# Kernel tuning notes

Hardware: AMD Instinct MI355X
Metric: run time of the kernel (lower is better)

## Reference

```python
import jax, jax.numpy as jnp
import numpy as np

T, B = 32, 64
D_IN = 512      # input_size == embedding dim
H = 512         # hidden_size
V = 32000       # n_vocab
F_FEAT = 768    # feature_size
NH = 8          # num_heads
HD = H // NH    # head_dim


def setup_inputs() -> dict:
    key = jax.random.key(0)
    ks = jax.random.split(key, 16)
    s = 0.02
    inp = {
        'y': jax.random.randint(ks[0], (T, B), 0, V),
        'ctx': jax.random.normal(ks[1], (1, B, F_FEAT), jnp.float32),
        'emb_W': jax.random.normal(ks[2], (V, D_IN), jnp.float32) * s,
        # GRUCell dec0: gates ordered (r, z, n) as in torch
        'W_ih': jax.random.normal(ks[3], (3 * H, D_IN), jnp.float32) * s,
        'b_ih': jnp.zeros((3 * H,), jnp.float32),
        'W_hh': jax.random.normal(ks[4], (3 * H, H), jnp.float32) * s,
        'b_hh': jnp.zeros((3 * H,), jnp.float32),
        # FF att: feature_size -> hidden, tanh
        'W_att': jax.random.normal(ks[5], (H, F_FEAT), jnp.float32) * s,
        'b_att': jnp.zeros((H,), jnp.float32),
        # MultiHeadSelfAttention projections (hidden -> hidden)
        'Wq': jax.random.normal(ks[6], (H, H), jnp.float32) * s,
        'bq': jnp.zeros((H,), jnp.float32),
        'Wk': jax.random.normal(ks[7], (H, H), jnp.float32) * s,
        'bk': jnp.zeros((H,), jnp.float32),
        'Wv': jax.random.normal(ks[8], (H, H), jnp.float32) * s,
        'bv': jnp.zeros((H,), jnp.float32),
        'Wfc': jax.random.normal(ks[9], (H, H), jnp.float32) * s,
        'bfc': jnp.zeros((H,), jnp.float32),
        # FF hid2out: hidden -> input, tanh, bias_zero
        'W_h2o': jax.random.normal(ks[10], (D_IN, H), jnp.float32) * s,
        'b_h2o': jnp.zeros((D_IN,), jnp.float32),
        # FF out2prob: input -> vocab, linear
        'W_out': jax.random.normal(ks[11], (V, D_IN), jnp.float32) * s,
        'b_out': jnp.zeros((V,), jnp.float32),
    }
    return inp


def reference(y, ctx, emb_W, W_ih, b_ih, W_hh, b_hh, W_att, b_att,
              Wq, bq, Wk, bk, Wv, bv, Wfc, bfc, W_h2o, b_h2o, W_out, b_out):
    y_emb = emb_W[y]                                   # [T, B, D_IN]
    # ct is constant across decode steps: tanh FF over pooled image feature
    ct = jnp.tanh(ctx[0] @ W_att.T + b_att)            # [B, H]
    h0 = jnp.zeros((y.shape[1], H), y_emb.dtype)       # dec_init 'zero'

    def step(h, y_t):
        # torch GRUCell (gate order r, z, n)
        gi = y_t @ W_ih.T + b_ih                       # [B, 3H]
        gh = h @ W_hh.T + b_hh                         # [B, 3H]
        gi_r, gi_z, gi_n = jnp.split(gi, 3, axis=-1)
        gh_r, gh_z, gh_n = jnp.split(gh, 3, axis=-1)
        r = jax.nn.sigmoid(gi_r + gh_r)
        z = jax.nn.sigmoid(gi_z + gh_z)
        n = jnp.tanh(gi_n + r * gh_n)
        h1 = (1.0 - z) * n + z * h                     # [B, H]

        x = h1 * ct                                    # [B, H]
        # MultiHeadSelfAttention on a single vector, heads act as sequence
        q = (x @ Wq.T + bq).reshape(-1, NH, HD)        # [B, NH, HD]
        k = (x @ Wk.T + bk).reshape(-1, NH, HD)
        v = (x @ Wv.T + bv).reshape(-1, NH, HD)
        scores = jnp.einsum('bhd,bgd->bhg', q, k) / HD  # note: /head_dim (not sqrt)
        attw = jax.nn.softmax(scores, axis=-1)
        att_out = jnp.einsum('bhg,bgd->bhd', attw, v).reshape(-1, H)
        h2 = att_out @ Wfc.T + bfc                     # [B, H] (fc_out, vocab_size==H)

        logit = jnp.tanh(h2 @ W_h2o.T + b_h2o)         # [B, D_IN]
        prob = jax.nn.softmax(logit @ W_out.T + b_out, axis=-1)  # [B, V]
        return h1, prob                                # f_next returns h1 as next state

    _, probs = jax.lax.scan(step, h0, y_emb)           # [T, B, V]
    return probs
```

## Files before the change

### kernel.cpp

```cpp
#include <hip/hip_runtime.h>
#include <hip/hip_bf16.h>
#include <math.h>

typedef __bf16 bf16_t;
typedef __bf16 bf16x8 __attribute__((ext_vector_type(8)));
typedef __bf16 bf16x4 __attribute__((ext_vector_type(4)));
typedef float  f32x4  __attribute__((ext_vector_type(4)));

#define T_STEPS 32
#define BATCH   64
#define DIN     512
#define HID     512
#define VOCAB   32000
#define FFEAT   768
#define ROWS    2048
#define G3      1536
#define NBLK_A  32

#define EPI_F32  0
#define EPI_BF16 1
#define EPI_TANH 2

#define GLOAD16(gp, lp) __builtin_amdgcn_global_load_lds( \
    (const __attribute__((address_space(1))) void*)(gp),  \
    (__attribute__((address_space(3))) void*)(lp), 16, 0, 0)

#define PHASEV(BUF, MH, NH, STAGE_STMT, GATE_STMT)                            \
  {                                                                           \
    bf16x8 af_[8], bf_[4];                                                    \
    _Pragma("unroll")                                                         \
    for (int m2 = 0; m2 < 4; ++m2) {                                          \
      const int row = wm * 64 + m2 * 16 + la;                                 \
      _Pragma("unroll")                                                       \
      for (int ks = 0; ks < 2; ++ks) {                                        \
        const int sl = (ks * 4 + lg) ^ (row & 7);                             \
        af_[m2 * 2 + ks] =                                                    \
            *(const bf16x8*)&lds[((BUF)*4 + (MH)) * 8192 + row * 64 + sl * 8];\
      }                                                                       \
    }                                                                         \
    _Pragma("unroll")                                                         \
    for (int n2 = 0; n2 < 2; ++n2) {                                          \
      const int row = wn * 32 + n2 * 16 + la;                                 \
      _Pragma("unroll")                                                       \
      for (int ks = 0; ks < 2; ++ks) {                                        \
        const int sl = (ks * 4 + lg) ^ (row & 7);                             \
        bf_[n2 * 2 + ks] =                                                    \
            *(const bf16x8*)&lds[((BUF)*4 + 2 + (NH)) * 8192 + row * 64 + sl * 8];\
      }                                                                       \
    }                                                                         \
    STAGE_STMT;                                                               \
    GATE_STMT;                                                                \
    __builtin_amdgcn_s_barrier();                                             \
    __builtin_amdgcn_s_setprio(1);                                            \
    _Pragma("unroll")                                                         \
    for (int m2 = 0; m2 < 4; ++m2)                                            \
      _Pragma("unroll")                                                       \
      for (int n2 = 0; n2 < 2; ++n2)                                          \
        _Pragma("unroll")                                                     \
        for (int ks = 0; ks < 2; ++ks)                                        \
          acc[(MH)*4 + m2][(NH)*2 + n2] =                                     \
              __builtin_amdgcn_mfma_f32_16x16x32_bf16(                        \
                  af_[m2*2+ks], bf_[n2*2+ks],                                 \
                  acc[(MH)*4 + m2][(NH)*2 + n2], 0, 0, 0);                    \
    __builtin_amdgcn_s_setprio(0);                                            \
    __builtin_amdgcn_s_barrier();                                             \
  }

template<int KD>
__global__ __launch_bounds__(512, 2) void gemm_v(
    const bf16_t* __restrict__ A, const bf16_t* __restrict__ B,
    const float* __restrict__ bias, bf16_t* __restrict__ ecache,
    float* __restrict__ partial, int M, int N, int NB)
{
  __shared__ bf16_t lds[2 * 4 * 8192];
  __shared__ float psum[256][4];
  const int tid = threadIdx.x;
  const int lane = tid & 63, wv = tid >> 6;
  const int wm = wv >> 2, wn = wv & 3;
  const int la = lane & 15, lg = lane >> 4;

  const int lin = blockIdx.x;
  const int mt = M >> 8;
  const int cpx = (NB * mt) >> 3;
  const int wg = (lin & 7) * cpx + (lin >> 3);
  const int bn = wg / mt, bm = wg - bn * mt;

  auto stageA = [&](int buf, int h, int kt) {
    const size_t base = (size_t)(bm * 256 + h * 128) * KD + (size_t)kt * 64;
#pragma unroll
    for (int q = 0; q < 2; ++q) {
      const int L = q * 512 + tid;
      const int row = L >> 3, sl = L & 7;
      const int c = sl ^ (row & 7);
      GLOAD16(A + base + (size_t)row * KD + c * 8,
              &lds[(buf * 4 + h) * 8192 + L * 8]);
    }
  };
  auto stageB = [&](int buf, int h, int kt) {
    const size_t base = (size_t)(bn * 256 + h * 128) * KD + (size_t)kt * 64;
#pragma unroll
    for (int q = 0; q < 2; ++q) {
      const int L = q * 512 + tid;
      const int row = L >> 3, sl = L & 7;
      const int c = sl ^ (row & 7);
      GLOAD16(B + base + (size_t)row * KD + c * 8,
              &lds[(buf * 4 + 2 + h) * 8192 + L * 8]);
    }
  };

  f32x4 acc[8][4] = {};
  constexpr int NITER = KD >> 7;

  stageA(0, 0, 0); stageB(0, 0, 0); stageA(0, 1, 0); stageB(0, 1, 0);
  stageA(1, 0, 1); stageB(1, 0, 1);
  asm volatile("s_waitcnt vmcnt(4)" ::: "memory");
  __builtin_amdgcn_s_barrier();

#pragma unroll
  for (int it = 0; it < NITER; ++it) {
    const int t0 = 2 * it;
    const bool lastI = (it == NITER - 1);
    PHASEV(0, 0, 0, { stageA(1, 1, t0 + 1); }, ;)
    PHASEV(0, 0, 1, { stageB(1, 1, t0 + 1); }, ;)
    PHASEV(0, 1, 0, { if (!lastI) stageA(0, 0, t0 + 2); }, ;)
    PHASEV(0, 1, 1, { if (!lastI) stageB(0, 0, t0 + 2); },
           { if (lastI) { asm volatile("s_waitcnt vmcnt(0)" ::: "memory"); }
             else       { asm volatile("s_waitcnt vmcnt(4)" ::: "memory"); } })
    PHASEV(1, 0, 0, { if (!lastI) stageA(0, 1, t0 + 2); }, ;)
    PHASEV(1, 0, 1, { if (!lastI) stageB(0, 1, t0 + 2); }, ;)
    PHASEV(1, 1, 0, { if (!lastI) stageA(1, 0, t0 + 3); }, ;)
    PHASEV(1, 1, 1, { if (!lastI) stageB(1, 0, t0 + 3); },
           { if (!lastI) { asm volatile("s_waitcnt vmcnt(4)" ::: "memory"); } })
  }

  float bv[4];
#pragma unroll
  for (int nj = 0; nj < 4; ++nj) {
    const int col = bn * 256 + (nj >> 1) * 128 + wn * 32 + (nj & 1) * 16 + la;
    bv[nj] = bias[col];
  }
#pragma unroll
  for (int mi = 0; mi < 8; ++mi) {
#pragma unroll
    for (int rr = 0; rr < 4; ++rr) {
      const int rowl = (mi >> 2) * 128 + wm * 64 + (mi & 3) * 16 + lg * 4 + rr;
      const int row = bm * 256 + rowl;
      float vsum = 0.f;
#pragma unroll
      for (int nj = 0; nj < 4; ++nj) {
        const float e = expf(acc[mi][nj][rr] + bv[nj]);
        const int col = bn * 256 + (nj >> 1) * 128 + wn * 32 + (nj & 1) * 16 + la;
        ecache[(size_t)row * N + col] = (bf16_t)e;
        vsum += e;
      }
      vsum += __shfl_xor(vsum, 1);
      vsum += __shfl_xor(vsum, 2);
      vsum += __shfl_xor(vsum, 4);
      vsum += __shfl_xor(vsum, 8);
      if (la == 0) psum[rowl][wn] = vsum;
    }
  }
  __syncthreads();
  if (tid < 256) {
    partial[(size_t)(bm * 256 + tid) * NB + bn] =
        psum[tid][0] + psum[tid][1] + psum[tid][2] + psum[tid][3];
  }
}

template<int EPI, int KD>
__global__ __launch_bounds__(256) void gemm_lds(
    const bf16_t* __restrict__ A, const bf16_t* __restrict__ B,
    const float* __restrict__ bias, void* __restrict__ out, int M, int N)
{
  __shared__ bf16_t As[3][128 * 32];
  __shared__ bf16_t Bs[3][128 * 32];

  const int lane = threadIdx.x & 63;
  const int wv   = threadIdx.x >> 6;
  const int wm = wv >> 1, wn = wv & 1;
  const int bn = blockIdx.x, bm = blockIdx.y;
  const int la = lane & 15, lg = lane >> 4;
  const int tid = threadIdx.x;

  auto stage = [&](int buf, int k0) {
#pragma unroll
    for (int q = 0; q < 2; ++q) {
      const int idx = q * 256 + tid;
      const int row = idx >> 2, c = idx & 3;
      const int gch = c ^ ((row >> 1) & 3);
      GLOAD16(A + (size_t)(bm * 128 + row) * KD + k0 + gch * 8, &As[buf][idx * 8]);
      GLOAD16(B + (size_t)(bn * 128 + row) * KD + k0 + gch * 8, &Bs[buf][idx * 8]);
    }
  };
  const int rdch = (lg ^ ((la >> 1) & 3)) * 8;

  f32x4 acc[4][4] = {};
  constexpr int NT = KD >> 5;
  stage(0, 0);
  stage(1, 32);
  for (int kt = 0; kt < NT; ++kt) {
    if (kt + 1 < NT) {
      asm volatile("s_waitcnt vmcnt(4)" ::: "memory");
    } else {
      asm volatile("s_waitcnt vmcnt(0)" ::: "memory");
    }
    __builtin_amdgcn_s_barrier();
    __builtin_amdgcn_sched_barrier(0);
    if (kt + 2 < NT) stage((kt + 2) % 3, (kt + 2) * 32);
    const bf16_t* Ab = As[kt % 3];
    const bf16_t* Bb = Bs[kt % 3];
    bf16x8 a[4], b[4];
#pragma unroll
    for (int i = 0; i < 4; ++i)
      a[i] = *(const bf16x8*)(Ab + (wm * 64 + i * 16 + la) * 32 + rdch);
#pragma unroll
    for (int j = 0; j < 4; ++j)
      b[j] = *(const bf16x8*)(Bb + (wn * 64 + j * 16 + la) * 32 + rdch);
    __builtin_amdgcn_s_setprio(1);
#pragma unroll
    for (int i = 0; i < 4; ++i)
#pragma unroll
      for (int j = 0; j < 4; ++j)
        acc[i][j] = __builtin_amdgcn_mfma_f32_16x16x32_bf16(a[i], b[j], acc[i][j], 0, 0, 0);
    __builtin_amdgcn_s_setprio(0);
  }

  const int m0 = bm * 128 + wm * 64;
  const int n0 = bn * 128 + wn * 64;
  float bv4[4];
#pragma unroll
  for (int j = 0; j < 4; ++j) bv4[j] = bias[n0 + j * 16 + la];
#pragma unroll
  for (int i = 0; i < 4; ++i) {
#pragma unroll
    for (int r = 0; r < 4; ++r) {
      const int row = m0 + i * 16 + lg * 4 + r;
#pragma unroll
      for (int j = 0; j < 4; ++j) {
        const int col = n0 + j * 16 + la;
        float v = acc[i][j][r] + bv4[j];
        if constexpr (EPI == EPI_F32) {
          ((float*)out)[(size_t)row * N + col] = v;
        } else if constexpr (EPI == EPI_BF16) {
          ((bf16_t*)out)[(size_t)row * N + col] = (bf16_t)v;
        } else {
          ((bf16_t*)out)[(size_t)row * N + col] = (bf16_t)tanhf(v);
        }
      }
    }
  }
}

__global__ __launch_bounds__(256) void phaseA_k(
    const bf16_t* __restrict__ Wg, const float* __restrict__ bhh,
    const float* __restrict__ gi, const float* __restrict__ ct,
    unsigned int* __restrict__ hbuf, bf16_t* __restrict__ Xall,
    int* __restrict__ flags, const float* __restrict__ Wout_f32,
    bf16_t* __restrict__ WoutB)
{
  __shared__ bf16_t Wl[48 * 520];
  __shared__ float bl[48];
  const int tid = threadIdx.x, blk = blockIdx.x;

  if (blk >= NBLK_A) {
    const int NCB = gridDim.x - NBLK_A;
    const int n4 = VOCAB * DIN / 4;
    for (int i = (blk - NBLK_A) * 256 + tid; i < n4; i += NCB * 256) {
      float4 v = ((const float4*)Wout_f32)[i];
      bf16x4 o = {(bf16_t)v.x, (bf16_t)v.y, (bf16_t)v.z, (bf16_t)v.w};
      *(bf16x4*)(WoutB + (size_t)i * 4) = o;
    }
    return;
  }

  for (int i = tid; i < 48 * 64; i += 256) {
    const int rw = i >> 6, ch = (i & 63) << 3;
    *(bf16x8*)(Wl + rw * 520 + ch) = *(const bf16x8*)(Wg + (size_t)(blk * 48 + rw) * 512 + ch);
  }
  if (tid < 48) bl[tid] = bhh[blk * 48 + tid];
  __syncthreads();

  const int lane = tid & 63, wv = tid >> 6;
  const int la = lane & 15, lg = lane >> 4;
  const int jcol = blk * 16 + la;
  const int rowA = wv * 16 + la;

  const float blr = bl[la], blz = bl[16 + la], bln = bl[32 + la];
  float hprev[4], ctv[4];
#pragma unroll
  for (int r = 0; r < 4; ++r) {
    hprev[r] = 0.f;
    ctv[r] = ct[(size_t)(wv * 16 + lg * 4 + r) * HID + jcol];
  }

  for (int t = 0; t < T_STEPS; ++t) {
    const float* girow = gi + (size_t)t * BATCH * G3 + (size_t)blk * 48;
    float gv[12];
#pragma unroll
    for (int r = 0; r < 4; ++r) {
      const float* gp = girow + (size_t)(wv * 16 + lg * 4 + r) * G3;
      gv[r * 3 + 0] = gp[la];
      gv[r * 3 + 1] = gp[16 + la];
      gv[r * 3 + 2] = gp[32 + la];
    }
    if (t > 0) {
      if (lane < 32) {
        while (__hip_atomic_load(&flags[(lane * 4 + wv) * 16], __ATOMIC_RELAXED,
                                 __HIP_MEMORY_SCOPE_AGENT) < t) { }
      }
      asm volatile("" ::: "memory");
    }
    const unsigned long long* hb =
        (const unsigned long long*)(hbuf + (size_t)(t & 1) * 16384);
    bf16x8 af[16];
#pragma unroll
    for (int q = 0; q < 16; ++q) {
      union { unsigned long long u[2]; bf16x8 v; } c;
      const size_t bidx = (size_t)(2 * q + (lg >> 1)) * 256 + rowA * 4 + (lg & 1) * 2;
      c.u[0] = __hip_atomic_load(hb + bidx,     __ATOMIC_RELAXED, __HIP_MEMORY_SCOPE_AGENT);
      c.u[1] = __hip_atomic_load(hb + bidx + 1, __ATOMIC_RELAXED, __HIP_MEMORY_SCOPE_AGENT);
      af[q] = c.v;
    }
    f32x4 acc0 = {}, acc1 = {}, acc2 = {};
#pragma unroll
    for (int q = 0; q < 16; ++q) {
      const bf16_t* wp = Wl + q * 32 + lg * 8;
      bf16x8 b0 = *(const bf16x8*)(wp + (0 * 16 + la) * 520);
      bf16x8 b1 = *(const bf16x8*)(wp + (1 * 16 + la) * 520);
      bf16x8 b2 = *(const bf16x8*)(wp + (2 * 16 + la) * 520);
      acc0 = __builtin_amdgcn_mfma_f32_16x16x32_bf16(af[q], b0, acc0, 0, 0, 0);
      acc1 = __builtin_amdgcn_mfma_f32_16x16x32_bf16(af[q], b1, acc1, 0, 0, 0);
      acc2 = __builtin_amdgcn_mfma_f32_16x16x32_bf16(af[q], b2, acc2, 0, 0, 0);
    }
    float h1v[4];
#pragma unroll
    for (int r = 0; r < 4; ++r) {
      const float ghr = acc0[r] + blr;
      const float ghz = acc1[r] + blz;
      const float ghn = acc2[r] + bln;
      const float rr = 1.f / (1.f + expf(-(gv[r * 3 + 0] + ghr)));
      const float zz = 1.f / (1.f + expf(-(gv[r * 3 + 1] + ghz)));
      const float nn = tanhf(gv[r * 3 + 2] + rr * ghn);
      h1v[r] = (1.f - zz) * nn + zz * hprev[r];
      hprev[r] = h1v[r];
    }
    unsigned int* hn = hbuf + (size_t)((t + 1) & 1) * 16384 + blk * 512;
#pragma unroll
    for (int r = 0; r < 4; ++r) {
      const int row = wv * 16 + lg * 4 + r;
      const unsigned int mine =
          (unsigned int)__builtin_bit_cast(unsigned short, (bf16_t)h1v[r]);
      const unsigned int other = (unsigned int)__shfl_xor((int)mine, 1);
      if ((la & 1) == 0) {
        __hip_atomic_store(hn + row * 8 + (la >> 1), mine | (other << 16),
                           __ATOMIC_RELAXED, __HIP_MEMORY_SCOPE_AGENT);
      }
    }
    asm volatile("s_waitcnt vmcnt(0)" ::: "memory");
    if (lane == 0) {
      __hip_atomic_store(&flags[(blk * 4 + wv) * 16], t + 1, __ATOMIC_RELAXED,
                         __HIP_MEMORY_SCOPE_AGENT);
    }
#pragma unroll
    for (int r = 0; r < 4; ++r) {
      const int row = wv * 16 + lg * 4 + r;
      Xall[((size_t)t * BATCH + row) * HID + jcol] = (bf16_t)(h1v[r] * ctv[r]);
    }
  }
}

__global__ __launch_bounds__(256) void attn_k(const bf16_t* __restrict__ QKV,
                                              bf16_t* __restrict__ attO)
{
  __shared__ float sq[4][512], sk[4][512], sv[4][512], sw[4][64];
  const int tid = threadIdx.x;
  const int wv = tid >> 6, lane = tid & 63;
  const int row = blockIdx.x * 4 + wv;
  const bf16_t* base = QKV + (size_t)row * G3;
  bf16x8 vq = *(const bf16x8*)(base + lane * 8);
  bf16x8 vk = *(const bf16x8*)(base + 512 + lane * 8);
  bf16x8 vv = *(const bf16x8*)(base + 1024 + lane * 8);
#pragma unroll
  for (int e = 0; e < 8; ++e) {
    sq[wv][lane * 8 + e] = (float)vq[e];
    sk[wv][lane * 8 + e] = (float)vk[e];
    sv[wv][lane * 8 + e] = (float)vv[e];
  }
  __syncthreads();
  const int h = lane >> 3, g = lane & 7;
  float s = 0.f;
#pragma unroll 16
  for (int d = 0; d < 64; ++d) s += sq[wv][h * 64 + d] * sk[wv][g * 64 + d];
  s *= (1.f / 64.f);
  float m = s;
  m = fmaxf(m, __shfl_xor(m, 1));
  m = fmaxf(m, __shfl_xor(m, 2));
  m = fmaxf(m, __shfl_xor(m, 4));
  const float e = expf(s - m);
  float sum = e;
  sum += __shfl_xor(sum, 1);
  sum += __shfl_xor(sum, 2);
  sum += __shfl_xor(sum, 4);
  sw[wv][lane] = e / sum;
  __syncthreads();
#pragma unroll
  for (int rep = 0; rep < 8; ++rep) {
    const int idx = rep * 64 + lane;
    const int hh = idx >> 6, d = idx & 63;
    float o = 0.f;
#pragma unroll
    for (int gg = 0; gg < 8; ++gg) o += sw[wv][hh * 8 + gg] * sv[wv][gg * 64 + d];
    attO[(size_t)row * HID + idx] = (bf16_t)o;
  }
}

__global__ __launch_bounds__(256) void cast5_k(
    const float* __restrict__ s0, const float* __restrict__ s1,
    const float* __restrict__ s2, const float* __restrict__ s3,
    const float* __restrict__ s4, bf16_t* __restrict__ Wqkv,
    bf16_t* __restrict__ WfcB, bf16_t* __restrict__ Wh2oB)
{
  const int seg = blockIdx.x >> 8;
  const int i = (blockIdx.x & 255) * 256 + threadIdx.x;
  const float* src = seg == 0 ? s0 : seg == 1 ? s1 : seg == 2 ? s2
                   : seg == 3 ? s3 : s4;
  bf16_t* dst = seg <= 2 ? Wqkv + (size_t)seg * HID * DIN
              : seg == 3 ? WfcB : Wh2oB;
  float4 v = ((const float4*)src)[i];
  bf16x4 o = {(bf16_t)v.x, (bf16_t)v.y, (bf16_t)v.z, (bf16_t)v.w};
  *(bf16x4*)(dst + (size_t)i * 4) = o;
}

__global__ __launch_bounds__(256) void perm_cast_k(const float* __restrict__ src,
                                                   bf16_t* __restrict__ dst)
{
  const int i = blockIdx.x * 256 + threadIdx.x;
  const int pg = i >> 7, kq = (i & 127) << 2;
  const int g = pg / 48, rem = pg - g * 48, sec = rem >> 4, jj = rem & 15;
  const int srow = sec * 512 + g * 16 + jj;
  float4 v = *(const float4*)(src + (size_t)srow * DIN + kq);
  bf16x4 o = {(bf16_t)v.x, (bf16_t)v.y, (bf16_t)v.z, (bf16_t)v.w};
  *(bf16x4*)(dst + (size_t)pg * DIN + kq) = o;
}

__global__ void perm_bias_k(const float* __restrict__ bih, const float* __restrict__ bhh,
                            float* __restrict__ bihp, float* __restrict__ bhhp)
{
  const int pg = blockIdx.x * 256 + threadIdx.x;
  if (pg >= G3) return;
  const int g = pg / 48, rem = pg - g * 48, sec = rem >> 4, jj = rem & 15;
  const int srow = sec * 512 + g * 16 + jj;
  bihp[pg] = bih[srow];
  bhhp[pg] = bhh[srow];
}

__global__ void bcat_k(const float* __restrict__ a, const float* __restrict__ b,
                       const float* __restrict__ c, float* __restrict__ d)
{
  const int i = blockIdx.x * 256 + threadIdx.x;
  if (i >= G3) return;
  d[i] = i < 512 ? a[i] : (i < 1024 ? b[i - 512] : c[i - 1024]);
}

__global__ __launch_bounds__(256) void yemb_k(const int* __restrict__ y,
                                              const float* __restrict__ embW,
                                              bf16_t* __restrict__ out)
{
  const int idx = blockIdx.x * 256 + threadIdx.x;
  const int rb = idx >> 6, c = (idx & 63) << 3;
  const int tok = y[rb];
  const float4* s = (const float4*)(embW + (size_t)tok * DIN + c);
  float4 v0 = s[0], v1 = s[1];
  bf16x8 o = {(bf16_t)v0.x, (bf16_t)v0.y, (bf16_t)v0.z, (bf16_t)v0.w,
              (bf16_t)v1.x, (bf16_t)v1.y, (bf16_t)v1.z, (bf16_t)v1.w};
  *(bf16x8*)(out + (size_t)rb * DIN + c) = o;
}

__global__ __launch_bounds__(256) void ct_k(const float* __restrict__ ctx,
                                            const float* __restrict__ Watt,
                                            const float* __restrict__ batt,
                                            float* __restrict__ ct)
{
  const int idx = blockIdx.x * 256 + threadIdx.x;
  const int b = idx >> 9, j = idx & 511;
  const float4* c4 = (const float4*)(ctx + (size_t)b * FFEAT);
  const float4* w4 = (const float4*)(Watt + (size_t)j * FFEAT);
  float s = batt[j];
  for (int q = 0; q < FFEAT / 4; ++q) {
    float4 cc = c4[q], ww = w4[q];
    s += cc.x * ww.x + cc.y * ww.y + cc.z * ww.z + cc.w * ww.w;
  }
  ct[idx] = tanhf(s);
}

__global__ __launch_bounds__(256) void reduce_rows(const float* __restrict__ partial,
                                                   float* __restrict__ rowsum, int NB)
{
  const int wv = threadIdx.x >> 6, lane = threadIdx.x & 63;
  const int row = blockIdx.x * 4 + wv;
  float s = 0.f;
  for (int c = lane; c < NB; c += 64) s += partial[(size_t)row * NB + c];
  for (int m = 1; m < 64; m <<= 1) s += __shfl_xor(s, m);
  if (lane == 0) rowsum[row] = s;
}

__global__ __launch_bounds__(256) void normalize_k(const bf16_t* __restrict__ e,
                                                   const float* __restrict__ rowsum,
                                                   float* __restrict__ out)
{
  const int row = blockIdx.y;
  const int c8 = blockIdx.x * 256 + threadIdx.x;
  if (c8 >= VOCAB / 8) return;
  const float inv = 1.0f / rowsum[row];
  const size_t base = (size_t)row * VOCAB + (size_t)c8 * 8;
  bf16x8 v = *(const bf16x8*)(e + base);
  float4 o0 = {(float)v[0] * inv, (float)v[1] * inv, (float)v[2] * inv, (float)v[3] * inv};
  float4 o1 = {(float)v[4] * inv, (float)v[5] * inv, (float)v[6] * inv, (float)v[7] * inv};
  *(float4*)(out + base) = o0;
  *(float4*)(out + base + 4) = o1;
}

extern "C" void kernel_launch(void* const* d_in, const int* in_sizes, int n_in,
                              void* d_out, int out_size, void* d_ws, size_t ws_size,
                              hipStream_t stream)
{
  const int*   y     = (const int*)  d_in[0];
  const float* ctx   = (const float*)d_in[1];
  const float* embW  = (const float*)d_in[2];
  const float* W_ih  = (const float*)d_in[3];
  const float* b_ih  = (const float*)d_in[4];
  const float* W_hh  = (const float*)d_in[5];
  const float* b_hh  = (const float*)d_in[6];
  const float* W_att = (const float*)d_in[7];
  const float* b_att = (const float*)d_in[8];
  const float* Wq    = (const float*)d_in[9];
  const float* bq    = (const float*)d_in[10];
  const float* Wk    = (const float*)d_in[11];
  const float* bk    = (const float*)d_in[12];
  const float* Wv    = (const float*)d_in[13];
  const float* bv    = (const float*)d_in[14];
  const float* Wfc   = (const float*)d_in[15];
  const float* bfc   = (const float*)d_in[16];
  const float* Wh2o  = (const float*)d_in[17];
  const float* bh2o  = (const float*)d_in[18];
  const float* W_out = (const float*)d_in[19];
  const float* b_out = (const float*)d_in[20];

  char* p = (char*)d_ws;
  auto alloc = [&](size_t bytes) {
    char* r = p;
    p += (bytes + 255) & ~(size_t)255;
    return r;
  };
  bf16_t* WoutB   = (bf16_t*)alloc((size_t)VOCAB * DIN * 2);
  bf16_t* WgIh    = (bf16_t*)alloc((size_t)G3 * DIN * 2);
  bf16_t* WgHh    = (bf16_t*)alloc((size_t)G3 * DIN * 2);
  bf16_t* Wqkv    = (bf16_t*)alloc((size_t)G3 * DIN * 2);
  bf16_t* WfcB    = (bf16_t*)alloc((size_t)HID * HID * 2);
  bf16_t* Wh2oB   = (bf16_t*)alloc((size_t)HID * HID * 2);
  float*  bIhP    = (float*)alloc(G3 * 4);
  float*  bHhP    = (float*)alloc(G3 * 4);
  float*  bQkv    = (float*)alloc(G3 * 4);
  bf16_t* Yemb    = (bf16_t*)alloc((size_t)ROWS * DIN * 2);
  float*  giP     = (float*)alloc((size_t)ROWS * G3 * 4);
  float*  ctB     = (float*)alloc((size_t)BATCH * HID * 4);
  unsigned int* hbuf = (unsigned int*)alloc((size_t)2 * 16384 * 4);
  bf16_t* Xall    = (bf16_t*)alloc((size_t)ROWS * DIN * 2);
  bf16_t* QKV     = (bf16_t*)alloc((size_t)ROWS * G3 * 2);
  bf16_t* attO    = (bf16_t*)alloc((size_t)ROWS * HID * 2);
  bf16_t* h2B     = (bf16_t*)alloc((size_t)ROWS * HID * 2);
  bf16_t* logit   = (bf16_t*)alloc((size_t)ROWS * DIN * 2);
  float*  partial = (float*)alloc((size_t)ROWS * 125 * 4);
  float*  rowsum  = (float*)alloc((size_t)ROWS * 4);
  int*    flags   = (int*)alloc(32 * 4 * 64);
  bf16_t* eCache  = (bf16_t*)alloc((size_t)ROWS * VOCAB * 2);

  hipMemsetAsync(hbuf, 0, (size_t)2 * 16384 * 4, stream);
  hipMemsetAsync(flags, 0, 32 * 4 * 64, stream);

  cast5_k<<<1280, 256, 0, stream>>>(Wq, Wk, Wv, Wfc, Wh2o, Wqkv, WfcB, Wh2oB);
  perm_cast_k<<<768, 256, 0, stream>>>(W_ih, WgIh);
  perm_cast_k<<<768, 256, 0, stream>>>(W_hh, WgHh);
  perm_bias_k<<<6, 256, 0, stream>>>(b_ih, b_hh, bIhP, bHhP);
  bcat_k<<<6, 256, 0, stream>>>(bq, bk, bv, bQkv);
  yemb_k<<<512, 256, 0, stream>>>(y, embW, Yemb);
  ct_k<<<128, 256, 0, stream>>>(ctx, W_att, b_att, ctB);

  gemm_lds<EPI_F32, DIN><<<dim3(12, 16), 256, 0, stream>>>(
      Yemb, WgIh, bIhP, giP, ROWS, G3);

  phaseA_k<<<224, 256, 0, stream>>>(WgHh, bHhP, giP, ctB, hbuf, Xall, flags,
                                    W_out, WoutB);

  gemm_lds<EPI_BF16, DIN><<<dim3(12, 16), 256, 0, stream>>>(
      Xall, Wqkv, bQkv, QKV, ROWS, G3);

  attn_k<<<512, 256, 0, stream>>>(QKV, attO);

  gemm_lds<EPI_BF16, HID><<<dim3(4, 16), 256, 0, stream>>>(
      attO, WfcB, bfc, h2B, ROWS, HID);

  gemm_lds<EPI_TANH, HID><<<dim3(4, 16), 256, 0, stream>>>(
      h2B, Wh2oB, bh2o, logit, ROWS, DIN);

  gemm_v<DIN><<<1000, 512, 0, stream>>>(
      logit, WoutB, b_out, eCache, partial, ROWS, VOCAB, 125);
  reduce_rows<<<512, 256, 0, stream>>>(partial, rowsum, 125);
  normalize_k<<<dim3(16, ROWS), 256, 0, stream>>>(eCache, rowsum, (float*)d_out);
}
```

Before: 442.2 us.

## Stage softmax exp tile through swizzled LDS for coalesced stores; split W_out cast

The vocab GEMM epilogue used to write scalar bf16 exp values straight to global memory. It now packs lane pairs via shuffles into a swizzled LDS tile and writes 16-byte coalesced rows. Separately, the W_out fp32->bf16 cast moves out of the extra blocks of the recurrent phaseA kernel into its own kernel launched up front, so phaseA runs only its 32 recurrent blocks. This adds LDS traffic, a sync and extra shuffles in exchange, and the cast no longer overlaps with the serial recurrence.

Result: slower. 502.9 us (+13.7%).

```diff
diff --git a/kernel.cpp b/kernel.cpp
--- a/kernel.cpp
+++ b/kernel.cpp
@@ -139,19 +139,29 @@
     const int col = bn * 256 + (nj >> 1) * 128 + wn * 32 + (nj & 1) * 16 + la;
     bv[nj] = bias[col];
   }
+  unsigned int* ldsw = (unsigned int*)lds;
+  const int odd = la & 1;
 #pragma unroll
   for (int mi = 0; mi < 8; ++mi) {
 #pragma unroll
     for (int rr = 0; rr < 4; ++rr) {
       const int rowl = (mi >> 2) * 128 + wm * 64 + (mi & 3) * 16 + lg * 4 + rr;
-      const int row = bm * 256 + rowl;
       float vsum = 0.f;
 #pragma unroll
       for (int nj = 0; nj < 4; ++nj) {
         const float e = expf(acc[mi][nj][rr] + bv[nj]);
-        const int col = bn * 256 + (nj >> 1) * 128 + wn * 32 + (nj & 1) * 16 + la;
-        ecache[(size_t)row * N + col] = (bf16_t)e;
         vsum += e;
+        const unsigned int mine =
+            (unsigned int)__builtin_bit_cast(unsigned short, (bf16_t)e);
+        const unsigned int other = (unsigned int)__shfl_xor((int)mine, 1);
+        if ((odd == 0) == (rr < 2)) {
+          const unsigned int pk = odd ? (other | (mine << 16))
+                                      : (mine | (other << 16));
+          const int cloc = (nj >> 1) * 128 + wn * 32 + (nj & 1) * 16 + (la & ~1);
+          const int cw = cloc >> 1;
+          const int phys = (cw >> 2) ^ ((rowl & 7) << 2);
+          ldsw[rowl * 128 + phys * 4 + (cw & 3)] = pk;
+        }
       }
       vsum += __shfl_xor(vsum, 1);
       vsum += __shfl_xor(vsum, 2);
@@ -161,6 +171,14 @@
     }
   }
   __syncthreads();
+#pragma unroll
+  for (int i = 0; i < 16; ++i) {
+    const int rowl = (tid >> 5) * 16 + i;
+    const int c16 = tid & 31;
+    const int phys = c16 ^ ((rowl & 7) << 2);
+    bf16x8 v = *(const bf16x8*)&lds[rowl * 256 + phys * 8];
+    *(bf16x8*)&ecache[(size_t)(bm * 256 + rowl) * N + bn * 256 + c16 * 8] = v;
+  }
   if (tid < 256) {
     partial[(size_t)(bm * 256 + tid) * NB + bn] =
         psum[tid][0] + psum[tid][1] + psum[tid][2] + psum[tid][3];
@@ -255,23 +273,11 @@
     const bf16_t* __restrict__ Wg, const float* __restrict__ bhh,
     const float* __restrict__ gi, const float* __restrict__ ct,
     unsigned int* __restrict__ hbuf, bf16_t* __restrict__ Xall,
-    int* __restrict__ flags, const float* __restrict__ Wout_f32,
-    bf16_t* __restrict__ WoutB)
+    int* __restrict__ flags)
 {
   __shared__ bf16_t Wl[48 * 520];
   __shared__ float bl[48];
   const int tid = threadIdx.x, blk = blockIdx.x;
-
-  if (blk >= NBLK_A) {
-    const int NCB = gridDim.x - NBLK_A;
-    const int n4 = VOCAB * DIN / 4;
-    for (int i = (blk - NBLK_A) * 256 + tid; i < n4; i += NCB * 256) {
-      float4 v = ((const float4*)Wout_f32)[i];
-      bf16x4 o = {(bf16_t)v.x, (bf16_t)v.y, (bf16_t)v.z, (bf16_t)v.w};
-      *(bf16x4*)(WoutB + (size_t)i * 4) = o;
-    }
-    return;
-  }
 
   for (int i = tid; i < 48 * 64; i += 256) {
     const int rw = i >> 6, ch = (i & 63) << 3;
@@ -412,6 +418,16 @@
     for (int gg = 0; gg < 8; ++gg) o += sw[wv][hh * 8 + gg] * sv[wv][gg * 64 + d];
     attO[(size_t)row * HID + idx] = (bf16_t)o;
   }
+}
+
+__global__ __launch_bounds__(256) void cast_k(const float* __restrict__ src,
+                                              bf16_t* __restrict__ dst, int n4)
+{
+  const int i = blockIdx.x * 256 + threadIdx.x;
+  if (i >= n4) return;
+  float4 v = ((const float4*)src)[i];
+  bf16x4 o = {(bf16_t)v.x, (bf16_t)v.y, (bf16_t)v.z, (bf16_t)v.w};
+  *(bf16x4*)(dst + (size_t)i * 4) = o;
 }
 
 __global__ __launch_bounds__(256) void cast5_k(
@@ -578,6 +594,7 @@
   hipMemsetAsync(hbuf, 0, (size_t)2 * 16384 * 4, stream);
   hipMemsetAsync(flags, 0, 32 * 4 * 64, stream);
 
+  cast_k<<<VOCAB * DIN / 4 / 256, 256, 0, stream>>>(W_out, WoutB, VOCAB * DIN / 4);
   cast5_k<<<1280, 256, 0, stream>>>(Wq, Wk, Wv, Wfc, Wh2o, Wqkv, WfcB, Wh2oB);
   perm_cast_k<<<768, 256, 0, stream>>>(W_ih, WgIh);
   perm_cast_k<<<768, 256, 0, stream>>>(W_hh, WgHh);
@@ -589,8 +606,7 @@
   gemm_lds<EPI_F32, DIN><<<dim3(12, 16), 256, 0, stream>>>(
       Yemb, WgIh, bIhP, giP, ROWS, G3);
 
-  phaseA_k<<<224, 256, 0, stream>>>(WgHh, bHhP, giP, ctB, hbuf, Xall, flags,
-                                    W_out, WoutB);
+  phaseA_k<<<NBLK_A, 256, 0, stream>>>(WgHh, bHhP, giP, ctB, hbuf, Xall, flags);
 
   gemm_lds<EPI_BF16, DIN><<<dim3(12, 16), 256, 0, stream>>>(
       Xall, Wqkv, bQkv, QKV, ROWS, G3);
```

## Split GEMM phases along K instead of N and pair bf16 stores

Applied to the files above, without the earlier changes.

The vocab-projection GEMM main loop now splits each LDS buffer into per-K-slice phases covering all four N subtiles, instead of per-N-half phases spanning both K slices. The global-to-LDS staging schedule and vmcnt waits are reordered to match: B halves are staged earlier and waits drop from 4 to 2 outstanding loads. The exp epilogue now packs two neighbouring bf16 outputs through a lane shuffle and writes them as one 32-bit store from even lanes, halving the store instruction count. The new staging order changes which loads can still be in flight at each barrier, which is a correctness risk if the wait counts are wrong.

Result: slower. 455.4 us (+3.0%).

```diff
diff --git a/kernel.cpp b/kernel.cpp
--- a/kernel.cpp
+++ b/kernel.cpp
@@ -25,28 +25,22 @@
     (const __attribute__((address_space(1))) void*)(gp),  \
     (__attribute__((address_space(3))) void*)(lp), 16, 0, 0)
 
-#define PHASEV(BUF, MH, NH, STAGE_STMT, GATE_STMT)                            \
+#define PHASEK(BUF, MH, KS, STAGE_STMT, GATE_STMT)                            \
   {                                                                           \
-    bf16x8 af_[8], bf_[4];                                                    \
+    bf16x8 af_[4], bf_[4];                                                    \
     _Pragma("unroll")                                                         \
     for (int m2 = 0; m2 < 4; ++m2) {                                          \
       const int row = wm * 64 + m2 * 16 + la;                                 \
-      _Pragma("unroll")                                                       \
-      for (int ks = 0; ks < 2; ++ks) {                                        \
-        const int sl = (ks * 4 + lg) ^ (row & 7);                             \
-        af_[m2 * 2 + ks] =                                                    \
-            *(const bf16x8*)&lds[((BUF)*4 + (MH)) * 8192 + row * 64 + sl * 8];\
-      }                                                                       \
+      const int sl = ((KS) * 4 + lg) ^ (row & 7);                             \
+      af_[m2] =                                                               \
+          *(const bf16x8*)&lds[((BUF)*4 + (MH)) * 8192 + row * 64 + sl * 8];  \
     }                                                                         \
     _Pragma("unroll")                                                         \
-    for (int n2 = 0; n2 < 2; ++n2) {                                          \
-      const int row = wn * 32 + n2 * 16 + la;                                 \
-      _Pragma("unroll")                                                       \
-      for (int ks = 0; ks < 2; ++ks) {                                        \
-        const int sl = (ks * 4 + lg) ^ (row & 7);                             \
-        bf_[n2 * 2 + ks] =                                                    \
-            *(const bf16x8*)&lds[((BUF)*4 + 2 + (NH)) * 8192 + row * 64 + sl * 8];\
-      }                                                                       \
+    for (int nj = 0; nj < 4; ++nj) {                                          \
+      const int row = wn * 32 + (nj & 1) * 16 + la;                           \
+      const int sl = ((KS) * 4 + lg) ^ (row & 7);                             \
+      bf_[nj] =                                                               \
+          *(const bf16x8*)&lds[((BUF)*4 + 2 + (nj >> 1)) * 8192 + row * 64 + sl * 8];\
     }                                                                         \
     STAGE_STMT;                                                               \
     GATE_STMT;                                                                \
@@ -55,13 +49,10 @@
     _Pragma("unroll")                                                         \
     for (int m2 = 0; m2 < 4; ++m2)                                            \
       _Pragma("unroll")                                                       \
-      for (int n2 = 0; n2 < 2; ++n2)                                          \
-        _Pragma("unroll")                                                     \
-        for (int ks = 0; ks < 2; ++ks)                                        \
-          acc[(MH)*4 + m2][(NH)*2 + n2] =                                     \
-              __builtin_amdgcn_mfma_f32_16x16x32_bf16(                        \
-                  af_[m2*2+ks], bf_[n2*2+ks],                                 \
-                  acc[(MH)*4 + m2][(NH)*2 + n2], 0, 0, 0);                    \
+      for (int nj = 0; nj < 4; ++nj)                                          \
+        acc[(MH)*4 + m2][nj] =                                                \
+            __builtin_amdgcn_mfma_f32_16x16x32_bf16(                          \
+                af_[m2], bf_[nj], acc[(MH)*4 + m2][nj], 0, 0, 0);             \
     __builtin_amdgcn_s_setprio(0);                                            \
     __builtin_amdgcn_s_barrier();                                             \
   }
@@ -111,26 +102,26 @@
   f32x4 acc[8][4] = {};
   constexpr int NITER = KD >> 7;
 
-  stageA(0, 0, 0); stageB(0, 0, 0); stageA(0, 1, 0); stageB(0, 1, 0);
-  stageA(1, 0, 1); stageB(1, 0, 1);
-  asm volatile("s_waitcnt vmcnt(4)" ::: "memory");
+  stageA(0, 0, 0); stageA(0, 1, 0); stageB(0, 0, 0); stageB(0, 1, 0);
+  stageA(1, 0, 1);
+  asm volatile("s_waitcnt vmcnt(2)" ::: "memory");
   __builtin_amdgcn_s_barrier();
 
 #pragma unroll
   for (int it = 0; it < NITER; ++it) {
     const int t0 = 2 * it;
     const bool lastI = (it == NITER - 1);
-    PHASEV(0, 0, 0, { stageA(1, 1, t0 + 1); }, ;)
-    PHASEV(0, 0, 1, { stageB(1, 1, t0 + 1); }, ;)
-    PHASEV(0, 1, 0, { if (!lastI) stageA(0, 0, t0 + 2); }, ;)
-    PHASEV(0, 1, 1, { if (!lastI) stageB(0, 0, t0 + 2); },
+    PHASEK(0, 0, 0, { stageA(1, 1, t0 + 1); stageB(1, 0, t0 + 1); }, ;)
+    PHASEK(0, 0, 1, { stageB(1, 1, t0 + 1); }, ;)
+    PHASEK(0, 1, 0, { if (!lastI) stageA(0, 0, t0 + 2); }, ;)
+    PHASEK(0, 1, 1, { },
            { if (lastI) { asm volatile("s_waitcnt vmcnt(0)" ::: "memory"); }
-             else       { asm volatile("s_waitcnt vmcnt(4)" ::: "memory"); } })
-    PHASEV(1, 0, 0, { if (!lastI) stageA(0, 1, t0 + 2); }, ;)
-    PHASEV(1, 0, 1, { if (!lastI) stageB(0, 1, t0 + 2); }, ;)
-    PHASEV(1, 1, 0, { if (!lastI) stageA(1, 0, t0 + 3); }, ;)
-    PHASEV(1, 1, 1, { if (!lastI) stageB(1, 0, t0 + 3); },
-           { if (!lastI) { asm volatile("s_waitcnt vmcnt(4)" ::: "memory"); } })
+             else       { asm volatile("s_waitcnt vmcnt(2)" ::: "memory"); } })
+    PHASEK(1, 0, 0, { if (!lastI) { stageA(0, 1, t0 + 2); stageB(0, 0, t0 + 2); } }, ;)
+    PHASEK(1, 0, 1, { if (!lastI) stageB(0, 1, t0 + 2); }, ;)
+    PHASEK(1, 1, 0, { if (!lastI) stageA(1, 0, t0 + 3); }, ;)
+    PHASEK(1, 1, 1, { },
+           { if (!lastI) { asm volatile("s_waitcnt vmcnt(2)" ::: "memory"); } })
   }
 
   float bv[4];
@@ -139,6 +130,7 @@
     const int col = bn * 256 + (nj >> 1) * 128 + wn * 32 + (nj & 1) * 16 + la;
     bv[nj] = bias[col];
   }
+  const int odd = la & 1;
 #pragma unroll
   for (int mi = 0; mi < 8; ++mi) {
 #pragma unroll
@@ -149,9 +141,14 @@
 #pragma unroll
       for (int nj = 0; nj < 4; ++nj) {
         const float e = expf(acc[mi][nj][rr] + bv[nj]);
-        const int col = bn * 256 + (nj >> 1) * 128 + wn * 32 + (nj & 1) * 16 + la;
-        ecache[(size_t)row * N + col] = (bf16_t)e;
         vsum += e;
+        const unsigned int mine =
+            (unsigned int)__builtin_bit_cast(unsigned short, (bf16_t)e);
+        const unsigned int other = (unsigned int)__shfl_xor((int)mine, 1);
+        if (!odd) {
+          const int col = bn * 256 + (nj >> 1) * 128 + wn * 32 + (nj & 1) * 16 + la;
+          *(unsigned int*)&ecache[(size_t)row * N + col] = mine | (other << 16);
+        }
       }
       vsum += __shfl_xor(vsum, 1);
       vsum += __shfl_xor(vsum, 2);
```
